# Performance work log

Hardware: AMD Instinct MI355X
Metric: run time of the kernel (lower is better)

Reference implementation:

```python
import jax, jax.numpy as jnp
import numpy as np


def _node_layer(X, Z, adj_v, T, W, b, p):
    # d_e = (Z @ p^T): per-edge scalar; multiplier = T diag(d_e) T^T  (Nv,Nv)
    d = (Z @ p.T)[:, 0]
    mult = (T * d[None, :]) @ T.T
    n = mult.shape[0]
    idx = jnp.arange(n)
    M = mult.at[idx, idx].set(1.0)           # diagonal forced to 1
    A = M * adj_v
    A = A / jnp.max(A, axis=0, keepdims=True)  # column-max normalization
    return A @ (X @ W) + b, Z


def _edge_layer(X, Z, adj_e, T, W, b, p):
    # d_v = (X @ p^T): per-node scalar; multiplier = T^T diag(d_v) T  (Ne,Ne)
    d = (X @ p.T)[:, 0]
    mult = (T.T * d[None, :]) @ T
    n = mult.shape[0]
    idx = jnp.arange(n)
    M = mult.at[idx, idx].set(1.0)
    A = M * adj_e
    A = A / jnp.max(A, axis=0, keepdims=True)
    return X, A @ (Z @ W) + b


def setup_inputs() -> dict:
    key = jax.random.key(0)
    ks = jax.random.split(key, 16)
    B, Nv, Ne = 16, 1024, 2048
    Fv, Fe, H, C = 128, 64, 128, 16
    inp = {
        "X": jax.random.normal(ks[0], (B, Nv, Fv), jnp.float32),
        "Z": jax.random.normal(ks[1], (B, Ne, Fe), jnp.float32),
        "adj_e": jax.random.uniform(ks[2], (B, Ne, Ne), jnp.float32, 0.01, 1.0),
        "adj_v": jax.random.uniform(ks[3], (B, Nv, Nv), jnp.float32, 0.01, 1.0),
        "T": jax.random.uniform(ks[4], (B, Nv, Ne), jnp.float32),
        # gc1: node layer  nfeat_v -> nhid, p over edge features
        "W1": jax.random.normal(ks[5], (Fv, H), jnp.float32) * 0.05,
        "b1": jnp.zeros((H,), jnp.float32),
        "p1": jax.random.normal(ks[6], (1, Fe), jnp.float32),
        # gc2: edge layer  nfeat_e -> nfeat_e, p over node features (nhid)
        "W2": jax.random.normal(ks[7], (Fe, Fe), jnp.float32) * 0.05,
        "b2": jnp.zeros((Fe,), jnp.float32),
        "p2": jax.random.normal(ks[8], (1, H), jnp.float32),
        # gc3: node layer  nhid -> nclass
        "W3": jax.random.normal(ks[9], (H, C), jnp.float32) * 0.05,
        "b3": jnp.zeros((C,), jnp.float32),
        "p3": jax.random.normal(ks[10], (1, Fe), jnp.float32),
    }
    return inp


def reference(X, Z, adj_e, adj_v, T, W1, b1, p1, W2, b2, p2, W3, b3, p3):
    # dropout is identity in eval mode
    def single(x, z, ae, av, t):
        x1, z1 = _node_layer(x, z, av, t, W1, b1, p1)
        x1, z1 = jax.nn.relu(x1), jax.nn.relu(z1)
        x2, z2 = _edge_layer(x1, z1, ae, t, W2, b2, p2)
        x2, z2 = jax.nn.relu(x2), jax.nn.relu(z2)
        x3, _ = _node_layer(x2, z2, av, t, W3, b3, p3)
        return x3
    return jax.vmap(single)(X, Z, adj_e, adj_v, T)  # (B, Nv, nclass)
```

## Files before the change

kernel.cpp:

```cpp
#include <hip/hip_runtime.h>
#include <hip/hip_bf16.h>
#include <stdint.h>

#define DEVI __device__ __forceinline__

typedef __bf16 bf16x8_t __attribute__((ext_vector_type(8)));
typedef float f32x4_t __attribute__((ext_vector_type(4)));
typedef unsigned short u16;

static constexpr int NBATCH = 16;
static constexpr int NV = 1024;
static constexpr int NE = 2048;
static constexpr int FV = 128;
static constexpr int FE = 64;
static constexpr int HID = 128;
static constexpr int NCLS = 16;

DEVI u16 f2bf(float f) { __hip_bfloat16 h = __float2bfloat16(f); return *reinterpret_cast<u16*>(&h); }
DEVI float bf2f(u16 u) { union { unsigned int i; float f; } x; x.i = ((unsigned int)u) << 16; return x.f; }

DEVI void gload_lds16(const void* g, void* l) {
  __builtin_amdgcn_global_load_lds(
      (const __attribute__((address_space(1))) unsigned int*)g,
      (__attribute__((address_space(3))) unsigned int*)l, 16, 0, 0);
}

__global__ void k_transpose(const float* __restrict__ T, u16* __restrict__ Tbf,
                            u16* __restrict__ Ttbf) {
  __shared__ u16 s[32][33];
  const int b = blockIdx.z;
  const int e0 = blockIdx.x * 32, v0 = blockIdx.y * 32;
  const float* Tb = T + (size_t)b * NV * NE;
  u16* T1 = Tbf + (size_t)b * NV * NE;
  u16* T2 = Ttbf + (size_t)b * NE * NV;
  const int tx = threadIdx.x & 31, ty = threadIdx.x >> 5;
  #pragma unroll
  for (int i = 0; i < 4; ++i) {
    int v = v0 + ty + i * 8;
    u16 u = f2bf(Tb[(size_t)v * NE + e0 + tx]);
    T1[(size_t)v * NE + e0 + tx] = u;
    s[ty + i * 8][tx] = u;
  }
  __syncthreads();
  #pragma unroll
  for (int i = 0; i < 4; ++i) {
    int e = e0 + ty + i * 8;
    T2[(size_t)e * NV + v0 + tx] = s[tx][ty + i * 8];
  }
}

__global__ void k_rowdot(const float* __restrict__ In, const float* __restrict__ p,
                         float* __restrict__ d, int R, int C) {
  const int b = blockIdx.y;
  const int w = threadIdx.x >> 6, l = threadIdx.x & 63;
  const int r = blockIdx.x * 4 + w;
  const float* row = In + ((size_t)b * R + r) * C;
  float s = 0.f;
  for (int c = l; c < C; c += 64) s += row[c] * p[c];
  #pragma unroll
  for (int o = 32; o; o >>= 1) s += __shfl_xor(s, o);
  if (l == 0) d[(size_t)b * R + r] = s;
}

template <bool BFIN>
__global__ void k_scale(const void* __restrict__ In, const float* __restrict__ d,
                        u16* __restrict__ Out, int K, int b0) {
  const int bi = blockIdx.y, bg = b0 + bi;
  const size_t elems = (size_t)NV * NE;
  const size_t idx = ((size_t)blockIdx.x * 256 + threadIdx.x) * 8;
  const float* dd = d + (size_t)bg * K;
  const int k = (int)(idx & (size_t)(K - 1));
  float f[8];
  if (BFIN) {
    const u16* in = (const u16*)In + (size_t)bg * elems + idx;
    uint4 raw = *(const uint4*)in;
    f[0] = bf2f(raw.x & 0xffff); f[1] = bf2f(raw.x >> 16);
    f[2] = bf2f(raw.y & 0xffff); f[3] = bf2f(raw.y >> 16);
    f[4] = bf2f(raw.z & 0xffff); f[5] = bf2f(raw.z >> 16);
    f[6] = bf2f(raw.w & 0xffff); f[7] = bf2f(raw.w >> 16);
  } else {
    const float* in = (const float*)In + (size_t)bg * elems + idx;
    float4 a0 = *(const float4*)in, a1 = *(const float4*)(in + 4);
    f[0] = a0.x; f[1] = a0.y; f[2] = a0.z; f[3] = a0.w;
    f[4] = a1.x; f[5] = a1.y; f[6] = a1.z; f[7] = a1.w;
  }
  u16 o[8];
  #pragma unroll
  for (int t = 0; t < 8; ++t) o[t] = f2bf(f[t] * dd[k + t]);
  *(uint4*)((u16*)Out + (size_t)bi * elems + idx) = *(uint4*)o;
}

__global__ __launch_bounds__(512, 2) void k_gemm256(
    const u16* __restrict__ A, size_t sA, int ldA,
    const u16* __restrict__ Bm, size_t sB, int ldB,
    int M, int K,
    const float* __restrict__ adj, u16* __restrict__ Pout, int b0) {
  extern __shared__ char smem[];
  const int gx = gridDim.x, gy = gridDim.y;
  const int total = gx * gy * gridDim.z;
  int orig = blockIdx.x + gx * (blockIdx.y + gy * blockIdx.z);
  const int cpx = total >> 3;
  int swz = (orig & 7) * cpx + (orig >> 3);
  const int bx = swz % gx;
  const int by = (swz / gx) % gy;
  const int bi = swz / (gx * gy);
  const int bg = b0 + bi;

  const u16* Ab = A + (size_t)bi * sA;
  const u16* Bb = Bm + (size_t)bg * sB;
  const int tm = by * 256, tn = bx * 256;
  const int tid = threadIdx.x, wid = tid >> 6, l = tid & 63;
  const int wr = wid >> 2, wc = wid & 3;

  const int srow = tid >> 3;
  const int scol = (((tid & 7) ^ (srow & 7)) << 3);

  const int Lx = (l & 7) << 4;
  const int colb0 = (((l >> 4) << 4)) ^ Lx;
  const int colb1 = (64 + ((l >> 4) << 4)) ^ Lx;
  const int arowb = (wr * 128 + (l & 15)) * 128;
  const int browb = (wc * 64 + (l & 15)) * 128;

  auto stage = [&](int buf, int k0) {
    char* ab = smem + (buf << 16);
    char* bb = ab + 32768;
    #pragma unroll
    for (int ld2 = 0; ld2 < 4; ++ld2) {
      gload_lds16(Ab + (size_t)(tm + ld2 * 64 + srow) * ldA + (k0 + scol),
                  ab + ld2 * 8192 + tid * 16);
      gload_lds16(Bb + (size_t)(tn + ld2 * 64 + srow) * ldB + (k0 + scol),
                  bb + ld2 * 8192 + tid * 16);
    }
  };

  f32x4_t acc[8][4];
  const f32x4_t zv = {0.f, 0.f, 0.f, 0.f};
  #pragma unroll
  for (int m = 0; m < 8; ++m)
    #pragma unroll
    for (int n = 0; n < 4; ++n) acc[m][n] = zv;

  const int NT = K >> 6;
  stage(0, 0);
  __syncthreads();

  for (int kt = 0; kt < NT; ++kt) {
    const int buf = kt & 1;
    if (kt + 1 < NT) stage(buf ^ 1, (kt + 1) << 6);
    char* abase = smem + (buf << 16);
    char* bbase = abase + 32768;
    bf16x8_t af[4][2], bfr[4][2];
    #pragma unroll
    for (int m = 0; m < 4; ++m) {
      af[m][0] = *(const bf16x8_t*)(abase + arowb + m * 2048 + colb0);
      af[m][1] = *(const bf16x8_t*)(abase + arowb + m * 2048 + colb1);
    }
    #pragma unroll
    for (int n = 0; n < 2; ++n) {
      bfr[n][0] = *(const bf16x8_t*)(bbase + browb + n * 2048 + colb0);
      bfr[n][1] = *(const bf16x8_t*)(bbase + browb + n * 2048 + colb1);
    }
    __builtin_amdgcn_s_setprio(1);
    #pragma unroll
    for (int m = 0; m < 4; ++m)
      #pragma unroll
      for (int n = 0; n < 2; ++n)
        #pragma unroll
        for (int kk = 0; kk < 2; ++kk)
          acc[m][n] = __builtin_amdgcn_mfma_f32_16x16x32_bf16(af[m][kk], bfr[n][kk], acc[m][n], 0, 0, 0);
    __builtin_amdgcn_s_setprio(0);
    #pragma unroll
    for (int n = 2; n < 4; ++n) {
      bfr[n][0] = *(const bf16x8_t*)(bbase + browb + n * 2048 + colb0);
      bfr[n][1] = *(const bf16x8_t*)(bbase + browb + n * 2048 + colb1);
    }
    __builtin_amdgcn_s_setprio(1);
    #pragma unroll
    for (int m = 0; m < 4; ++m)
      #pragma unroll
      for (int n = 2; n < 4; ++n)
        #pragma unroll
        for (int kk = 0; kk < 2; ++kk)
          acc[m][n] = __builtin_amdgcn_mfma_f32_16x16x32_bf16(af[m][kk], bfr[n][kk], acc[m][n], 0, 0, 0);
    __builtin_amdgcn_s_setprio(0);
    #pragma unroll
    for (int m = 0; m < 4; ++m) {
      af[m][0] = *(const bf16x8_t*)(abase + arowb + (m + 4) * 2048 + colb0);
      af[m][1] = *(const bf16x8_t*)(abase + arowb + (m + 4) * 2048 + colb1);
    }
    __builtin_amdgcn_s_setprio(1);
    #pragma unroll
    for (int m = 0; m < 4; ++m)
      #pragma unroll
      for (int n = 2; n < 4; ++n)
        #pragma unroll
        for (int kk = 0; kk < 2; ++kk)
          acc[m + 4][n] = __builtin_amdgcn_mfma_f32_16x16x32_bf16(af[m][kk], bfr[n][kk], acc[m + 4][n], 0, 0, 0);
    __builtin_amdgcn_s_setprio(0);
    __builtin_amdgcn_s_setprio(1);
    #pragma unroll
    for (int m = 0; m < 4; ++m)
      #pragma unroll
      for (int n = 0; n < 2; ++n)
        #pragma unroll
        for (int kk = 0; kk < 2; ++kk)
          acc[m + 4][n] = __builtin_amdgcn_mfma_f32_16x16x32_bf16(af[m][kk], bfr[n][kk], acc[m + 4][n], 0, 0, 0);
    __builtin_amdgcn_s_setprio(0);
    __syncthreads();
  }

  const float* adjb = adj + (size_t)bg * M * M;
  u16* Pb = Pout + (size_t)bi * (size_t)M * M;
  #pragma unroll
  for (int m = 0; m < 8; ++m)
    #pragma unroll
    for (int n = 0; n < 4; ++n)
      #pragma unroll
      for (int q = 0; q < 4; ++q) {
        int row = tm + wr * 128 + m * 16 + (l >> 4) * 4 + q;
        int col = tn + wc * 64 + n * 16 + (l & 15);
        float v = acc[m][n][q];
        if (row == col) v = 1.0f;
        v *= adjb[(size_t)row * M + col];
        Pb[(size_t)row * M + col] = f2bf(v);
      }
}

template <int EPI>
__global__ __launch_bounds__(256) void k_gemm(
    const u16* __restrict__ A, size_t sA, int ldA,
    const u16* __restrict__ Bm, size_t sB, int ldB,
    int M, int K, int Nrows, int Ncols,
    const float* __restrict__ bias, float* __restrict__ Fout, int b0) {
  __shared__ __align__(16) u16 As[2][128 * 32];
  __shared__ __align__(16) u16 Bs[2][128 * 32];
  const int bi = blockIdx.z, bg = b0 + bi;
  const u16* Ab = A + (size_t)bi * sA;
  const u16* Bb = Bm + (size_t)bg * sB;
  const int tm = blockIdx.y * 128, tn = blockIdx.x * 128;
  const int tid = threadIdx.x, w = tid >> 6, l = tid & 63;
  const int wm = (w >> 1) * 64, wn = (w & 1) * 64;
  const int lr = l & 15, kg = (l >> 4) * 8;
  const int chunk = l & 3;
  int arow[2], brow[2];
  #pragma unroll
  for (int i = 0; i < 2; ++i) {
    int r = (i * 4 + w) * 16 + (l >> 2);
    arow[i] = tm + r;
    int rb = tn + r;
    brow[i] = rb < Nrows ? rb : Nrows - 1;
  }
  f32x4_t acc[4][4];
  const f32x4_t zv = {0.f, 0.f, 0.f, 0.f};
  #pragma unroll
  for (int m = 0; m < 4; ++m)
    #pragma unroll
    for (int n = 0; n < 4; ++n) acc[m][n] = zv;

  auto stage = [&](int buf, int k0) {
    #pragma unroll
    for (int i = 0; i < 2; ++i) {
      gload_lds16(Ab + (size_t)arow[i] * ldA + k0 + chunk * 8,
                  (char*)As[buf] + (i * 4 + w) * 1024);
      gload_lds16(Bb + (size_t)brow[i] * ldB + k0 + chunk * 8,
                  (char*)Bs[buf] + (i * 4 + w) * 1024);
    }
  };

  const int nsteps = K >> 5;
  stage(0, 0);
  __syncthreads();
  for (int s = 0; s < nsteps; ++s) {
    const int cur = s & 1;
    if (s + 1 < nsteps) stage(cur ^ 1, (s + 1) << 5);
    bf16x8_t af[4], bfr[4];
    #pragma unroll
    for (int m = 0; m < 4; ++m) af[m] = *(const bf16x8_t*)&As[cur][(wm + m * 16 + lr) * 32 + kg];
    #pragma unroll
    for (int n = 0; n < 4; ++n) bfr[n] = *(const bf16x8_t*)&Bs[cur][(wn + n * 16 + lr) * 32 + kg];
    #pragma unroll
    for (int m = 0; m < 4; ++m)
      #pragma unroll
      for (int n = 0; n < 4; ++n)
        acc[m][n] = __builtin_amdgcn_mfma_f32_16x16x32_bf16(af[m], bfr[n], acc[m][n], 0, 0, 0);
    __syncthreads();
  }

  float* Ob = Fout + (size_t)bg * M * Ncols;
  #pragma unroll
  for (int m = 0; m < 4; ++m)
    #pragma unroll
    for (int n = 0; n < 4; ++n)
      #pragma unroll
      for (int q = 0; q < 4; ++q) {
        int row = tm + wm + m * 16 + (l >> 4) * 4 + q;
        int col = tn + wn + n * 16 + lr;
        if (col < Ncols) {
          float v = acc[m][n][q] + bias[col];
          if (EPI == 1) v = fmaxf(v, 0.f);
          Ob[(size_t)row * Ncols + col] = v;
        }
      }
}

__global__ void k_colmax(const u16* __restrict__ P, unsigned int* __restrict__ c,
                         int M, int N, int rowsPer, int b0) {
  const int bi = blockIdx.z, bg = b0 + bi;
  const u16* Pb = P + (size_t)bi * (size_t)M * N;
  const int j = (blockIdx.x * 256 + threadIdx.x) * 4;
  const int r0 = blockIdx.y * rowsPer;
  float m0 = 0.f, m1 = 0.f, m2 = 0.f, m3 = 0.f;
  for (int i = r0; i < r0 + rowsPer; ++i) {
    uint2 v = *(const uint2*)(Pb + (size_t)i * N + j);
    m0 = fmaxf(m0, bf2f(v.x & 0xffff)); m1 = fmaxf(m1, bf2f(v.x >> 16));
    m2 = fmaxf(m2, bf2f(v.y & 0xffff)); m3 = fmaxf(m3, bf2f(v.y >> 16));
  }
  unsigned int* cb = c + (size_t)bg * N;
  atomicMax(cb + j + 0, __float_as_uint(m0));
  atomicMax(cb + j + 1, __float_as_uint(m1));
  atomicMax(cb + j + 2, __float_as_uint(m2));
  atomicMax(cb + j + 3, __float_as_uint(m3));
}

template <bool RELU_IN>
__global__ __launch_bounds__(256) void k_smallgemm(
    const float* __restrict__ X, size_t sX, int Kd,
    const float* __restrict__ W, int Cc,
    const float* __restrict__ cmax, u16* __restrict__ YT, size_t sY,
    int Nj, int b0) {
  __shared__ float Xs[64][129];
  __shared__ float Ws[128][33];
  const int bg = b0 + blockIdx.y;
  const float* Xb = X + (size_t)bg * sX;
  const int j0 = blockIdx.x * 64;
  const int tid = threadIdx.x;
  for (int idx = tid; idx < 64 * (Kd / 4); idx += 256) {
    int r = idx / (Kd / 4), q = idx % (Kd / 4);
    float4 v = *(const float4*)(Xb + (size_t)(j0 + r) * Kd + q * 4);
    if (RELU_IN) {
      v.x = fmaxf(v.x, 0.f); v.y = fmaxf(v.y, 0.f);
      v.z = fmaxf(v.z, 0.f); v.w = fmaxf(v.w, 0.f);
    }
    Xs[r][q * 4 + 0] = v.x; Xs[r][q * 4 + 1] = v.y;
    Xs[r][q * 4 + 2] = v.z; Xs[r][q * 4 + 3] = v.w;
  }
  const int r = tid & 63, cg = tid >> 6;
  const float rinv = 1.0f / cmax[(size_t)bg * Nj + j0 + r];
  for (int c0 = 0; c0 < Cc; c0 += 32) {
    __syncthreads();
    for (int idx = tid; idx < Kd * 32; idx += 256) {
      int k = idx >> 5, c = c0 + (idx & 31);
      Ws[k][idx & 31] = (c < Cc) ? W[(size_t)k * Cc + c] : 0.f;
    }
    __syncthreads();
    float acc[8] = {0.f, 0.f, 0.f, 0.f, 0.f, 0.f, 0.f, 0.f};
    for (int k = 0; k < Kd; ++k) {
      float xv = Xs[r][k];
      #pragma unroll
      for (int cc = 0; cc < 8; ++cc) acc[cc] += xv * Ws[k][cg * 8 + cc];
    }
    #pragma unroll
    for (int cc = 0; cc < 8; ++cc) {
      int c = c0 + cg * 8 + cc;
      if (c < Cc) YT[(size_t)bg * sY + (size_t)c * Nj + j0 + r] = f2bf(acc[cc] * rinv);
    }
  }
}

extern "C" void kernel_launch(void* const* d_in, const int* in_sizes, int n_in,
                              void* d_out, int out_size, void* d_ws, size_t ws_size,
                              hipStream_t stream) {
  const float* X    = (const float*)d_in[0];
  const float* Z    = (const float*)d_in[1];
  const float* adje = (const float*)d_in[2];
  const float* adjv = (const float*)d_in[3];
  const float* T    = (const float*)d_in[4];
  const float* W1   = (const float*)d_in[5];
  const float* b1   = (const float*)d_in[6];
  const float* p1   = (const float*)d_in[7];
  const float* W2   = (const float*)d_in[8];
  const float* b2   = (const float*)d_in[9];
  const float* p2   = (const float*)d_in[10];
  const float* W3   = (const float*)d_in[11];
  const float* b3   = (const float*)d_in[12];
  const float* p3   = (const float*)d_in[13];
  float* out = (float*)d_out;
  (void)in_sizes; (void)n_in; (void)out_size;

  hipFuncSetAttribute(reinterpret_cast<const void*>(k_gemm256),
                      hipFuncAttributeMaxDynamicSharedMemorySize, 131072);

  char* ws = (char*)d_ws;
  size_t off = 0;
  auto alloc = [&](size_t n) -> char* {
    char* p = ws + off; off = (off + n + 255) & ~(size_t)255; return p;
  };
  u16* Tbf    = (u16*)alloc((size_t)NBATCH * NV * NE * 2);
  u16* Ttbf   = (u16*)alloc((size_t)NBATCH * NE * NV * 2);
  float* dbuf = (float*)alloc((size_t)NBATCH * NE * 4);
  float* cbuf = (float*)alloc((size_t)NBATCH * NE * 4);
  u16* YT     = (u16*)alloc((size_t)NBATCH * NE * 64 * 2);
  float* x1   = (float*)alloc((size_t)NBATCH * NV * HID * 4);
  float* z2   = (float*)alloc((size_t)NBATCH * NE * FE * 4);
  const size_t needA = (size_t)NBATCH * NV * NE * 2;
  const size_t needP = (size_t)NBATCH * NE * NE * 2;
  const bool full = (ws_size >= off + needA + needP + 1024);
  const int nb = full ? NBATCH : 1;
  u16* Asc = (u16*)alloc(full ? needA : (size_t)NV * NE * 2);
  u16* P   = (u16*)alloc(full ? needP : (size_t)NE * NE * 2);

  const dim3 blk(256, 1, 1);
  const dim3 blk512(512, 1, 1);
  const size_t cbytes = (size_t)NBATCH * NE * 4;

  k_transpose<<<dim3(NE / 32, NV / 32, NBATCH), blk, 0, stream>>>(T, Tbf, Ttbf);

  k_rowdot<<<dim3(NE / 4, NBATCH), blk, 0, stream>>>(Z, p1, dbuf, NE, FE);
  for (int b0 = 0; b0 < NBATCH; b0 += nb) {
    k_scale<false><<<dim3((NV * NE) / 2048, nb), blk, 0, stream>>>(T, dbuf, Asc, NE, b0);
    k_gemm256<<<dim3(NV / 256, NV / 256, nb), blk512, 131072, stream>>>(
        Asc, (size_t)NV * NE, NE, Tbf, (size_t)NV * NE, NE, NV, NE, adjv, P, b0);
    hipMemsetAsync(cbuf, 0, cbytes, stream);
    k_colmax<<<dim3(NV / 1024, NV / 32, nb), blk, 0, stream>>>(
        P, (unsigned int*)cbuf, NV, NV, 32, b0);
    k_smallgemm<false><<<dim3(NV / 64, nb), blk, 0, stream>>>(
        X, (size_t)NV * FV, FV, W1, HID, cbuf, YT, (size_t)NV * HID, NV, b0);
    k_gemm<1><<<dim3(1, NV / 128, nb), blk, 0, stream>>>(
        P, (size_t)NV * NV, NV, YT, (size_t)NV * HID, NV,
        NV, NV, HID, HID, b1, x1, b0);
  }
  k_rowdot<<<dim3(NV / 4, NBATCH), blk, 0, stream>>>(x1, p2, dbuf, NV, HID);
  for (int b0 = 0; b0 < NBATCH; b0 += nb) {
    k_scale<true><<<dim3((NE * NV) / 2048, nb), blk, 0, stream>>>(Ttbf, dbuf, Asc, NV, b0);
    k_gemm256<<<dim3(NE / 256, NE / 256, nb), blk512, 131072, stream>>>(
        Asc, (size_t)NE * NV, NV, Ttbf, (size_t)NE * NV, NV, NE, NV, adje, P, b0);
    hipMemsetAsync(cbuf, 0, cbytes, stream);
    k_colmax<<<dim3(NE / 1024, NE / 64, nb), blk, 0, stream>>>(
        P, (unsigned int*)cbuf, NE, NE, 64, b0);
    k_smallgemm<true><<<dim3(NE / 64, nb), blk, 0, stream>>>(
        Z, (size_t)NE * FE, FE, W2, FE, cbuf, YT, (size_t)NE * FE, NE, b0);
    k_gemm<1><<<dim3(1, NE / 128, nb), blk, 0, stream>>>(
        P, (size_t)NE * NE, NE, YT, (size_t)NE * FE, NE,
        NE, NE, FE, FE, b2, z2, b0);
  }
  k_rowdot<<<dim3(NE / 4, NBATCH), blk, 0, stream>>>(z2, p3, dbuf, NE, FE);
  for (int b0 = 0; b0 < NBATCH; b0 += nb) {
    k_scale<false><<<dim3((NV * NE) / 2048, nb), blk, 0, stream>>>(T, dbuf, Asc, NE, b0);
    k_gemm256<<<dim3(NV / 256, NV / 256, nb), blk512, 131072, stream>>>(
        Asc, (size_t)NV * NE, NE, Tbf, (size_t)NV * NE, NE, NV, NE, adjv, P, b0);
    hipMemsetAsync(cbuf, 0, cbytes, stream);
    k_colmax<<<dim3(NV / 1024, NV / 32, nb), blk, 0, stream>>>(
        P, (unsigned int*)cbuf, NV, NV, 32, b0);
    k_smallgemm<false><<<dim3(NV / 64, nb), blk, 0, stream>>>(
        x1, (size_t)NV * HID, HID, W3, NCLS, cbuf, YT, (size_t)NV * NCLS, NV, b0);
    k_gemm<2><<<dim3(1, NV / 128, nb), blk, 0, stream>>>(
        P, (size_t)NV * NV, NV, YT, (size_t)NV * NCLS, NV,
        NV, NV, NCLS, NCLS, b3, out, b0);
  }
}
```

Baseline: 759.1 us.

## Split GEMM tile into quadrant phases with staged prefetch and fine-grained barriers

After: 734.9 us. 3.2% less time.

```diff
diff --git a/kernel.cpp b/kernel.cpp
--- a/kernel.cpp
+++ b/kernel.cpp
@@ -90,12 +90,38 @@
   *(uint4*)((u16*)Out + (size_t)bi * elems + idx) = *(uint4*)o;
 }
 
+#define LDA8(MH) \
+  _Pragma("unroll") \
+  for (int m = 0; m < 4; ++m) { \
+    const char* pA = abase + ((MH) * 128 + wr * 64 + m * 16 + lr) * 128; \
+    af[m][0] = *(const bf16x8_t*)(pA + colb0); \
+    af[m][1] = *(const bf16x8_t*)(pA + colb1); \
+  }
+#define LDB4(BF, NH) \
+  _Pragma("unroll") \
+  for (int n = 0; n < 2; ++n) { \
+    const char* pB = bbase + ((NH) * 128 + wc * 32 + n * 16 + lr) * 128; \
+    BF[n][0] = *(const bf16x8_t*)(pB + colb0); \
+    BF[n][1] = *(const bf16x8_t*)(pB + colb1); \
+  }
+#define MFMA_QUAD(MH, NH, BF) \
+  __builtin_amdgcn_s_setprio(1); \
+  _Pragma("unroll") \
+  for (int m = 0; m < 4; ++m) \
+    _Pragma("unroll") \
+    for (int n = 0; n < 2; ++n) \
+      _Pragma("unroll") \
+      for (int kk = 0; kk < 2; ++kk) \
+        acc[(MH) * 4 + m][(NH) * 2 + n] = __builtin_amdgcn_mfma_f32_16x16x32_bf16( \
+            af[m][kk], BF[n][kk], acc[(MH) * 4 + m][(NH) * 2 + n], 0, 0, 0); \
+  __builtin_amdgcn_s_setprio(0);
+
 __global__ __launch_bounds__(512, 2) void k_gemm256(
     const u16* __restrict__ A, size_t sA, int ldA,
     const u16* __restrict__ Bm, size_t sB, int ldB,
     int M, int K,
     const float* __restrict__ adj, u16* __restrict__ Pout, int b0) {
-  extern __shared__ char smem[];
+  extern __shared__ __align__(16) char smem[];
   const int gx = gridDim.x, gy = gridDim.y;
   const int total = gx * gy * gridDim.z;
   int orig = blockIdx.x + gx * (blockIdx.y + gy * blockIdx.z);
@@ -111,26 +137,22 @@
   const int tm = by * 256, tn = bx * 256;
   const int tid = threadIdx.x, wid = tid >> 6, l = tid & 63;
   const int wr = wid >> 2, wc = wid & 3;
-
-  const int srow = tid >> 3;
-  const int scol = (((tid & 7) ^ (srow & 7)) << 3);
-
+  const int lr = l & 15;
   const int Lx = (l & 7) << 4;
   const int colb0 = (((l >> 4) << 4)) ^ Lx;
   const int colb1 = (64 + ((l >> 4) << 4)) ^ Lx;
-  const int arowb = (wr * 128 + (l & 15)) * 128;
-  const int browb = (wc * 64 + (l & 15)) * 128;
-
-  auto stage = [&](int buf, int k0) {
-    char* ab = smem + (buf << 16);
-    char* bb = ab + 32768;
-    #pragma unroll
-    for (int ld2 = 0; ld2 < 4; ++ld2) {
-      gload_lds16(Ab + (size_t)(tm + ld2 * 64 + srow) * ldA + (k0 + scol),
-                  ab + ld2 * 8192 + tid * 16);
-      gload_lds16(Bb + (size_t)(tn + ld2 * 64 + srow) * ldB + (k0 + scol),
-                  bb + ld2 * 8192 + tid * 16);
-    }
+  const int srow = tid >> 3;
+  const int scol = (((tid & 7) ^ (srow & 7)) << 3);
+
+  auto stageA = [&](char* ab, int k0, int pa) {
+    const int rho = pa * 64 + srow;
+    const int row = ((rho >> 6) & 1) * 128 + (rho >> 7) * 64 + (rho & 63);
+    gload_lds16(Ab + (size_t)(tm + row) * ldA + (k0 + scol), ab + pa * 8192 + tid * 16);
+  };
+  auto stageB = [&](char* bb, int k0, int pb) {
+    const int rho = pb * 64 + srow;
+    const int row = ((rho >> 5) & 3) * 64 + (rho >> 7) * 32 + (rho & 31);
+    gload_lds16(Bb + (size_t)(tn + row) * ldB + (k0 + scol), bb + pb * 8192 + tid * 16);
   };
 
   f32x4_t acc[8][4];
@@ -139,74 +161,61 @@
   for (int m = 0; m < 8; ++m)
     #pragma unroll
     for (int n = 0; n < 4; ++n) acc[m][n] = zv;
+  bf16x8_t af[4][2], blo[2][2], bhi[2][2];
 
   const int NT = K >> 6;
-  stage(0, 0);
-  __syncthreads();
+  {
+    char* ab = smem; char* bb = smem + 32768;
+    stageA(ab, 0, 0); stageA(ab, 0, 1);
+    stageB(bb, 0, 0); stageB(bb, 0, 1);
+    stageB(bb, 0, 2); stageB(bb, 0, 3);
+    stageA(ab, 0, 2); stageA(ab, 0, 3);
+  }
+  asm volatile("s_waitcnt vmcnt(4)" ::: "memory");
+  __builtin_amdgcn_s_barrier();
 
   for (int kt = 0; kt < NT; ++kt) {
-    const int buf = kt & 1;
-    if (kt + 1 < NT) stage(buf ^ 1, (kt + 1) << 6);
-    char* abase = smem + (buf << 16);
+    char* abase = smem + ((kt & 1) << 16);
     char* bbase = abase + 32768;
-    bf16x8_t af[4][2], bfr[4][2];
-    #pragma unroll
-    for (int m = 0; m < 4; ++m) {
-      af[m][0] = *(const bf16x8_t*)(abase + arowb + m * 2048 + colb0);
-      af[m][1] = *(const bf16x8_t*)(abase + arowb + m * 2048 + colb1);
-    }
-    #pragma unroll
-    for (int n = 0; n < 2; ++n) {
-      bfr[n][0] = *(const bf16x8_t*)(bbase + browb + n * 2048 + colb0);
-      bfr[n][1] = *(const bf16x8_t*)(bbase + browb + n * 2048 + colb1);
-    }
-    __builtin_amdgcn_s_setprio(1);
-    #pragma unroll
-    for (int m = 0; m < 4; ++m)
-      #pragma unroll
-      for (int n = 0; n < 2; ++n)
-        #pragma unroll
-        for (int kk = 0; kk < 2; ++kk)
-          acc[m][n] = __builtin_amdgcn_mfma_f32_16x16x32_bf16(af[m][kk], bfr[n][kk], acc[m][n], 0, 0, 0);
-    __builtin_amdgcn_s_setprio(0);
-    #pragma unroll
-    for (int n = 2; n < 4; ++n) {
-      bfr[n][0] = *(const bf16x8_t*)(bbase + browb + n * 2048 + colb0);
-      bfr[n][1] = *(const bf16x8_t*)(bbase + browb + n * 2048 + colb1);
-    }
-    __builtin_amdgcn_s_setprio(1);
-    #pragma unroll
-    for (int m = 0; m < 4; ++m)
-      #pragma unroll
-      for (int n = 2; n < 4; ++n)
-        #pragma unroll
-        for (int kk = 0; kk < 2; ++kk)
-          acc[m][n] = __builtin_amdgcn_mfma_f32_16x16x32_bf16(af[m][kk], bfr[n][kk], acc[m][n], 0, 0, 0);
-    __builtin_amdgcn_s_setprio(0);
-    #pragma unroll
-    for (int m = 0; m < 4; ++m) {
-      af[m][0] = *(const bf16x8_t*)(abase + arowb + (m + 4) * 2048 + colb0);
-      af[m][1] = *(const bf16x8_t*)(abase + arowb + (m + 4) * 2048 + colb1);
-    }
-    __builtin_amdgcn_s_setprio(1);
-    #pragma unroll
-    for (int m = 0; m < 4; ++m)
-      #pragma unroll
-      for (int n = 2; n < 4; ++n)
-        #pragma unroll
-        for (int kk = 0; kk < 2; ++kk)
-          acc[m + 4][n] = __builtin_amdgcn_mfma_f32_16x16x32_bf16(af[m][kk], bfr[n][kk], acc[m + 4][n], 0, 0, 0);
-    __builtin_amdgcn_s_setprio(0);
-    __builtin_amdgcn_s_setprio(1);
-    #pragma unroll
-    for (int m = 0; m < 4; ++m)
-      #pragma unroll
-      for (int n = 0; n < 2; ++n)
-        #pragma unroll
-        for (int kk = 0; kk < 2; ++kk)
-          acc[m + 4][n] = __builtin_amdgcn_mfma_f32_16x16x32_bf16(af[m][kk], bfr[n][kk], acc[m + 4][n], 0, 0, 0);
-    __builtin_amdgcn_s_setprio(0);
-    __syncthreads();
+    char* nab = smem + (((kt & 1) ^ 1) << 16);
+    char* nbb = nab + 32768;
+    const int nk0 = (kt + 1) << 6;
+    const bool pre = (kt + 1 < NT);
+
+    LDA8(0);
+    LDB4(blo, 0);
+    if (pre) { stageA(nab, nk0, 0); stageA(nab, nk0, 1); }
+    __builtin_amdgcn_s_barrier();
+    asm volatile("s_waitcnt lgkmcnt(0)" ::: "memory");
+    __builtin_amdgcn_sched_barrier(0);
+    MFMA_QUAD(0, 0, blo);
+    if (pre) asm volatile("s_waitcnt vmcnt(4)" ::: "memory");
+    else     asm volatile("s_waitcnt vmcnt(2)" ::: "memory");
+    __builtin_amdgcn_s_barrier();
+
+    LDB4(bhi, 1);
+    if (pre) { stageB(nbb, nk0, 0); stageB(nbb, nk0, 1); }
+    __builtin_amdgcn_s_barrier();
+    asm volatile("s_waitcnt lgkmcnt(0)" ::: "memory");
+    __builtin_amdgcn_sched_barrier(0);
+    MFMA_QUAD(0, 1, bhi);
+    if (pre) asm volatile("s_waitcnt vmcnt(4)" ::: "memory");
+    else     asm volatile("s_waitcnt vmcnt(0)" ::: "memory");
+    __builtin_amdgcn_s_barrier();
+
+    LDA8(1);
+    if (pre) { stageB(nbb, nk0, 2); stageB(nbb, nk0, 3); }
+    __builtin_amdgcn_s_barrier();
+    asm volatile("s_waitcnt lgkmcnt(0)" ::: "memory");
+    __builtin_amdgcn_sched_barrier(0);
+    MFMA_QUAD(1, 0, blo);
+    __builtin_amdgcn_s_barrier();
+
+    if (pre) { stageA(nab, nk0, 2); stageA(nab, nk0, 3); }
+    __builtin_amdgcn_s_barrier();
+    MFMA_QUAD(1, 1, bhi);
+    if (pre) asm volatile("s_waitcnt vmcnt(4)" ::: "memory");
+    __builtin_amdgcn_s_barrier();
   }
 
   const float* adjb = adj + (size_t)bg * M * M;
@@ -417,7 +426,7 @@
 
   k_rowdot<<<dim3(NE / 4, NBATCH), blk, 0, stream>>>(Z, p1, dbuf, NE, FE);
   for (int b0 = 0; b0 < NBATCH; b0 += nb) {
-    k_scale<false><<<dim3((NV * NE) / 2048, nb), blk, 0, stream>>>(T, dbuf, Asc, NE, b0);
+    k_scale<true><<<dim3((NV * NE) / 2048, nb), blk, 0, stream>>>(Tbf, dbuf, Asc, NE, b0);
     k_gemm256<<<dim3(NV / 256, NV / 256, nb), blk512, 131072, stream>>>(
         Asc, (size_t)NV * NE, NE, Tbf, (size_t)NV * NE, NE, NV, NE, adjv, P, b0);
     hipMemsetAsync(cbuf, 0, cbytes, stream);
@@ -445,7 +454,7 @@
   }
   k_rowdot<<<dim3(NE / 4, NBATCH), blk, 0, stream>>>(z2, p3, dbuf, NE, FE);
   for (int b0 = 0; b0 < NBATCH; b0 += nb) {
-    k_scale<false><<<dim3((NV * NE) / 2048, nb), blk, 0, stream>>>(T, dbuf, Asc, NE, b0);
+    k_scale<true><<<dim3((NV * NE) / 2048, nb), blk, 0, stream>>>(Tbf, dbuf, Asc, NE, b0);
     k_gemm256<<<dim3(NV / 256, NV / 256, nb), blk512, 131072, stream>>>(
         Asc, (size_t)NV * NE, NE, Tbf, (size_t)NV * NE, NE, NV, NE, adjv, P, b0);
     hipMemsetAsync(cbuf, 0, cbytes, stream);
```

## Fuse column-max into GEMM epilogue and scaling into transpose, add narrow PY GEMM

Applied to the files above, without the earlier changes.

Result: faster. 659.7 us (-13.1%).

```diff
diff --git a/kernel.cpp b/kernel.cpp
--- a/kernel.cpp
+++ b/kernel.cpp
@@ -25,8 +25,10 @@
       (__attribute__((address_space(3))) unsigned int*)l, 16, 0, 0);
 }
 
+template <bool WRITE_ASC>
 __global__ void k_transpose(const float* __restrict__ T, u16* __restrict__ Tbf,
-                            u16* __restrict__ Ttbf) {
+                            u16* __restrict__ Ttbf, const float* __restrict__ d1,
+                            u16* __restrict__ Asc1) {
   __shared__ u16 s[32][33];
   const int b = blockIdx.z;
   const int e0 = blockIdx.x * 32, v0 = blockIdx.y * 32;
@@ -34,11 +36,15 @@
   u16* T1 = Tbf + (size_t)b * NV * NE;
   u16* T2 = Ttbf + (size_t)b * NE * NV;
   const int tx = threadIdx.x & 31, ty = threadIdx.x >> 5;
+  float dv = 0.f;
+  if (WRITE_ASC) dv = d1[(size_t)b * NE + e0 + tx];
   #pragma unroll
   for (int i = 0; i < 4; ++i) {
     int v = v0 + ty + i * 8;
-    u16 u = f2bf(Tb[(size_t)v * NE + e0 + tx]);
+    float f = Tb[(size_t)v * NE + e0 + tx];
+    u16 u = f2bf(f);
     T1[(size_t)v * NE + e0 + tx] = u;
+    if (WRITE_ASC) Asc1[(size_t)b * NV * NE + (size_t)v * NE + e0 + tx] = f2bf(f * dv);
     s[ty + i * 8][tx] = u;
   }
   __syncthreads();
@@ -62,28 +68,20 @@
   if (l == 0) d[(size_t)b * R + r] = s;
 }
 
-template <bool BFIN>
-__global__ void k_scale(const void* __restrict__ In, const float* __restrict__ d,
+__global__ void k_scale(const u16* __restrict__ In, const float* __restrict__ d,
                         u16* __restrict__ Out, int K, int b0) {
   const int bi = blockIdx.y, bg = b0 + bi;
   const size_t elems = (size_t)NV * NE;
   const size_t idx = ((size_t)blockIdx.x * 256 + threadIdx.x) * 8;
   const float* dd = d + (size_t)bg * K;
   const int k = (int)(idx & (size_t)(K - 1));
+  const u16* in = In + (size_t)bg * elems + idx;
+  uint4 raw = *(const uint4*)in;
   float f[8];
-  if (BFIN) {
-    const u16* in = (const u16*)In + (size_t)bg * elems + idx;
-    uint4 raw = *(const uint4*)in;
-    f[0] = bf2f(raw.x & 0xffff); f[1] = bf2f(raw.x >> 16);
-    f[2] = bf2f(raw.y & 0xffff); f[3] = bf2f(raw.y >> 16);
-    f[4] = bf2f(raw.z & 0xffff); f[5] = bf2f(raw.z >> 16);
-    f[6] = bf2f(raw.w & 0xffff); f[7] = bf2f(raw.w >> 16);
-  } else {
-    const float* in = (const float*)In + (size_t)bg * elems + idx;
-    float4 a0 = *(const float4*)in, a1 = *(const float4*)(in + 4);
-    f[0] = a0.x; f[1] = a0.y; f[2] = a0.z; f[3] = a0.w;
-    f[4] = a1.x; f[5] = a1.y; f[6] = a1.z; f[7] = a1.w;
-  }
+  f[0] = bf2f(raw.x & 0xffff); f[1] = bf2f(raw.x >> 16);
+  f[2] = bf2f(raw.y & 0xffff); f[3] = bf2f(raw.y >> 16);
+  f[4] = bf2f(raw.z & 0xffff); f[5] = bf2f(raw.z >> 16);
+  f[6] = bf2f(raw.w & 0xffff); f[7] = bf2f(raw.w >> 16);
   u16 o[8];
   #pragma unroll
   for (int t = 0; t < 8; ++t) o[t] = f2bf(f[t] * dd[k + t]);
@@ -94,8 +92,9 @@
     const u16* __restrict__ A, size_t sA, int ldA,
     const u16* __restrict__ Bm, size_t sB, int ldB,
     int M, int K,
-    const float* __restrict__ adj, u16* __restrict__ Pout, int b0) {
-  extern __shared__ char smem[];
+    const float* __restrict__ adj, u16* __restrict__ Pout,
+    float* __restrict__ pmax, int b0) {
+  extern __shared__ __align__(16) char smem[];
   const int gx = gridDim.x, gy = gridDim.y;
   const int total = gx * gy * gridDim.z;
   int orig = blockIdx.x + gx * (blockIdx.y + gy * blockIdx.z);
@@ -211,6 +210,7 @@
 
   const float* adjb = adj + (size_t)bg * M * M;
   u16* Pb = Pout + (size_t)bi * (size_t)M * M;
+  float vmax[4] = {0.f, 0.f, 0.f, 0.f};
   #pragma unroll
   for (int m = 0; m < 8; ++m)
     #pragma unroll
@@ -222,8 +222,39 @@
         float v = acc[m][n][q];
         if (row == col) v = 1.0f;
         v *= adjb[(size_t)row * M + col];
+        vmax[n] = fmaxf(vmax[n], v);
         Pb[(size_t)row * M + col] = f2bf(v);
       }
+  #pragma unroll
+  for (int n = 0; n < 4; ++n) {
+    vmax[n] = fmaxf(vmax[n], __shfl_xor(vmax[n], 16));
+    vmax[n] = fmaxf(vmax[n], __shfl_xor(vmax[n], 32));
+  }
+  float* red = (float*)smem;
+  if (l < 16) {
+    #pragma unroll
+    for (int n = 0; n < 4; ++n)
+      red[((wr * 4 + wc) * 4 + n) * 16 + l] = vmax[n];
+  }
+  __syncthreads();
+  if (wr == 0 && l < 16) {
+    #pragma unroll
+    for (int n = 0; n < 4; ++n) {
+      float a = red[((0 * 4 + wc) * 4 + n) * 16 + l];
+      float b = red[((1 * 4 + wc) * 4 + n) * 16 + l];
+      pmax[((size_t)bi * gy + by) * M + tn + wc * 64 + n * 16 + l] = fmaxf(a, b);
+    }
+  }
+}
+
+__global__ void k_colmax2(const float* __restrict__ pmax, float* __restrict__ c,
+                          int N, int G, int b0) {
+  const int bi = blockIdx.y, bg = b0 + bi;
+  const int j = blockIdx.x * 256 + threadIdx.x;
+  const float* pb = pmax + (size_t)bi * G * N;
+  float m = 0.f;
+  for (int g = 0; g < G; ++g) m = fmaxf(m, pb[(size_t)g * N + j]);
+  c[(size_t)bg * N + j] = m;
 }
 
 template <int EPI>
@@ -303,23 +334,77 @@
       }
 }
 
-__global__ void k_colmax(const u16* __restrict__ P, unsigned int* __restrict__ c,
-                         int M, int N, int rowsPer, int b0) {
+template <int EPI>
+__global__ __launch_bounds__(256) void k_gemmPY(
+    const u16* __restrict__ A, size_t sA, int ldA,
+    const u16* __restrict__ Bm, size_t sB,
+    int M, int K, int Ncols,
+    const float* __restrict__ bias, float* __restrict__ Fout, int b0) {
+  __shared__ __align__(16) u16 As[2][128 * 32];
+  __shared__ __align__(16) u16 Bs[2][64 * 32];
   const int bi = blockIdx.z, bg = b0 + bi;
-  const u16* Pb = P + (size_t)bi * (size_t)M * N;
-  const int j = (blockIdx.x * 256 + threadIdx.x) * 4;
-  const int r0 = blockIdx.y * rowsPer;
-  float m0 = 0.f, m1 = 0.f, m2 = 0.f, m3 = 0.f;
-  for (int i = r0; i < r0 + rowsPer; ++i) {
-    uint2 v = *(const uint2*)(Pb + (size_t)i * N + j);
-    m0 = fmaxf(m0, bf2f(v.x & 0xffff)); m1 = fmaxf(m1, bf2f(v.x >> 16));
-    m2 = fmaxf(m2, bf2f(v.y & 0xffff)); m3 = fmaxf(m3, bf2f(v.y >> 16));
-  }
-  unsigned int* cb = c + (size_t)bg * N;
-  atomicMax(cb + j + 0, __float_as_uint(m0));
-  atomicMax(cb + j + 1, __float_as_uint(m1));
-  atomicMax(cb + j + 2, __float_as_uint(m2));
-  atomicMax(cb + j + 3, __float_as_uint(m3));
+  const u16* Ab = A + (size_t)bi * sA;
+  const u16* Bb = Bm + (size_t)bg * sB;
+  const int tm = blockIdx.y * 128;
+  const int tid = threadIdx.x, w = tid >> 6, l = tid & 63;
+  const int wm = (w >> 1) * 64, wn = (w & 1) * 32;
+  const int lr = l & 15, kg = (l >> 4) * 8;
+  const int chunk = l & 3;
+  int arow[2];
+  #pragma unroll
+  for (int i = 0; i < 2; ++i) arow[i] = tm + (i * 4 + w) * 16 + (l >> 2);
+  const int brow = w * 16 + (l >> 2);
+
+  f32x4_t acc[4][2];
+  const f32x4_t zv = {0.f, 0.f, 0.f, 0.f};
+  #pragma unroll
+  for (int m = 0; m < 4; ++m)
+    #pragma unroll
+    for (int n = 0; n < 2; ++n) acc[m][n] = zv;
+
+  auto stage = [&](int buf, int k0) {
+    #pragma unroll
+    for (int i = 0; i < 2; ++i)
+      gload_lds16(Ab + (size_t)arow[i] * ldA + k0 + chunk * 8,
+                  (char*)As[buf] + (i * 4 + w) * 1024);
+    gload_lds16(Bb + (size_t)brow * ldA  + k0 + chunk * 8,
+                (char*)Bs[buf] + tid * 16);
+  };
+
+  const int nsteps = K >> 5;
+  stage(0, 0);
+  __syncthreads();
+  for (int s = 0; s < nsteps; ++s) {
+    const int cur = s & 1;
+    if (s + 1 < nsteps) stage(cur ^ 1, (s + 1) << 5);
+    bf16x8_t af[4], bfr[2];
+    #pragma unroll
+    for (int m = 0; m < 4; ++m) af[m] = *(const bf16x8_t*)&As[cur][(wm + m * 16 + lr) * 32 + kg];
+    #pragma unroll
+    for (int n = 0; n < 2; ++n) bfr[n] = *(const bf16x8_t*)&Bs[cur][(wn + n * 16 + lr) * 32 + kg];
+    #pragma unroll
+    for (int m = 0; m < 4; ++m)
+      #pragma unroll
+      for (int n = 0; n < 2; ++n)
+        acc[m][n] = __builtin_amdgcn_mfma_f32_16x16x32_bf16(af[m], bfr[n], acc[m][n], 0, 0, 0);
+    __syncthreads();
+  }
+
+  float* Ob = Fout + (size_t)bg * M * Ncols;
+  #pragma unroll
+  for (int m = 0; m < 4; ++m)
+    #pragma unroll
+    for (int n = 0; n < 2; ++n)
+      #pragma unroll
+      for (int q = 0; q < 4; ++q) {
+        int row = tm + wm + m * 16 + (l >> 4) * 4 + q;
+        int col = wn + n * 16 + lr;
+        if (col < Ncols) {
+          float v = acc[m][n][q] + bias[col];
+          if (EPI == 1) v = fmaxf(v, 0.f);
+          Ob[(size_t)row * Ncols + col] = v;
+        }
+      }
 }
 
 template <bool RELU_IN>
@@ -399,6 +484,7 @@
   u16* Ttbf   = (u16*)alloc((size_t)NBATCH * NE * NV * 2);
   float* dbuf = (float*)alloc((size_t)NBATCH * NE * 4);
   float* cbuf = (float*)alloc((size_t)NBATCH * NE * 4);
+  float* pmax = (float*)alloc((size_t)NBATCH * 8 * NE * 4);
   u16* YT     = (u16*)alloc((size_t)NBATCH * NE * 64 * 2);
   float* x1   = (float*)alloc((size_t)NBATCH * NV * HID * 4);
   float* z2   = (float*)alloc((size_t)NBATCH * NE * FE * 4);
@@ -411,18 +497,21 @@
 
   const dim3 blk(256, 1, 1);
   const dim3 blk512(512, 1, 1);
-  const size_t cbytes = (size_t)NBATCH * NE * 4;
-
-  k_transpose<<<dim3(NE / 32, NV / 32, NBATCH), blk, 0, stream>>>(T, Tbf, Ttbf);
 
   k_rowdot<<<dim3(NE / 4, NBATCH), blk, 0, stream>>>(Z, p1, dbuf, NE, FE);
+  if (full)
+    k_transpose<true><<<dim3(NE / 32, NV / 32, NBATCH), blk, 0, stream>>>(
+        T, Tbf, Ttbf, dbuf, Asc);
+  else
+    k_transpose<false><<<dim3(NE / 32, NV / 32, NBATCH), blk, 0, stream>>>(
+        T, Tbf, Ttbf, nullptr, nullptr);
+
   for (int b0 = 0; b0 < NBATCH; b0 += nb) {
-    k_scale<false><<<dim3((NV * NE) / 2048, nb), blk, 0, stream>>>(T, dbuf, Asc, NE, b0);
+    if (!full)
+      k_scale<<<dim3((NV * NE) / 2048, nb), blk, 0, stream>>>(Tbf, dbuf, Asc, NE, b0);
     k_gemm256<<<dim3(NV / 256, NV / 256, nb), blk512, 131072, stream>>>(
-        Asc, (size_t)NV * NE, NE, Tbf, (size_t)NV * NE, NE, NV, NE, adjv, P, b0);
-    hipMemsetAsync(cbuf, 0, cbytes, stream);
-    k_colmax<<<dim3(NV / 1024, NV / 32, nb), blk, 0, stream>>>(
-        P, (unsigned int*)cbuf, NV, NV, 32, b0);
+        Asc, (size_t)NV * NE, NE, Tbf, (size_t)NV * NE, NE, NV, NE, adjv, P, pmax, b0);
+    k_colmax2<<<dim3(NV / 256, nb), blk, 0, stream>>>(pmax, cbuf, NV, NV / 256, b0);
     k_smallgemm<false><<<dim3(NV / 64, nb), blk, 0, stream>>>(
         X, (size_t)NV * FV, FV, W1, HID, cbuf, YT, (size_t)NV * HID, NV, b0);
     k_gemm<1><<<dim3(1, NV / 128, nb), blk, 0, stream>>>(
@@ -431,30 +520,26 @@
   }
   k_rowdot<<<dim3(NV / 4, NBATCH), blk, 0, stream>>>(x1, p2, dbuf, NV, HID);
   for (int b0 = 0; b0 < NBATCH; b0 += nb) {
-    k_scale<true><<<dim3((NE * NV) / 2048, nb), blk, 0, stream>>>(Ttbf, dbuf, Asc, NV, b0);
+    k_scale<<<dim3((NE * NV) / 2048, nb), blk, 0, stream>>>(Ttbf, dbuf, Asc, NV, b0);
     k_gemm256<<<dim3(NE / 256, NE / 256, nb), blk512, 131072, stream>>>(
-        Asc, (size_t)NE * NV, NV, Ttbf, (size_t)NE * NV, NV, NE, NV, adje, P, b0);
-    hipMemsetAsync(cbuf, 0, cbytes, stream);
-    k_colmax<<<dim3(NE / 1024, NE / 64, nb), blk, 0, stream>>>(
-        P, (unsigned int*)cbuf, NE, NE, 64, b0);
+        Asc, (size_t)NE * NV, NV, Ttbf, (size_t)NE * NV, NV, NE, NV, adje, P, pmax, b0);
+    k_colmax2<<<dim3(NE / 256, nb), blk, 0, stream>>>(pmax, cbuf, NE, NE / 256, b0);
     k_smallgemm<true><<<dim3(NE / 64, nb), blk, 0, stream>>>(
         Z, (size_t)NE * FE, FE, W2, FE, cbuf, YT, (size_t)NE * FE, NE, b0);
-    k_gemm<1><<<dim3(1, NE / 128, nb), blk, 0, stream>>>(
-        P, (size_t)NE * NE, NE, YT, (size_t)NE * FE, NE,
-        NE, NE, FE, FE, b2, z2, b0);
+    k_gemmPY<1><<<dim3(1, NE / 128, nb), blk, 0, stream>>>(
+        P, (size_t)NE * NE, NE, YT, (size_t)NE * FE,
+        NE, NE, FE, b2, z2, b0);
   }
   k_rowdot<<<dim3(NE / 4, NBATCH), blk, 0, stream>>>(z2, p3, dbuf, NE, FE);
   for (int b0 = 0; b0 < NBATCH; b0 += nb) {
-    k_scale<false><<<dim3((NV * NE) / 2048, nb), blk, 0, stream>>>(T, dbuf, Asc, NE, b0);
+    k_scale<<<dim3((NV * NE) / 2048, nb), blk, 0, stream>>>(Tbf, dbuf, Asc, NE, b0);
     k_gemm256<<<dim3(NV / 256, NV / 256, nb), blk512, 131072, stream>>>(
-        Asc, (size_t)NV * NE, NE, Tbf, (size_t)NV * NE, NE, NV, NE, adjv, P, b0);
-    hipMemsetAsync(cbuf, 0, cbytes, stream);
-    k_colmax<<<dim3(NV / 1024, NV / 32, nb), blk, 0, stream>>>(
-        P, (unsigned int*)cbuf, NV, NV, 32, b0);
+        Asc, (size_t)NV * NE, NE, Tbf, (size_t)NV * NE, NE, NV, NE, adjv, P, pmax, b0);
+    k_colmax2<<<dim3(NV / 256, nb), blk, 0, stream>>>(pmax, cbuf, NV, NV / 256, b0);
     k_smallgemm<false><<<dim3(NV / 64, nb), blk, 0, stream>>>(
         x1, (size_t)NV * HID, HID, W3, NCLS, cbuf, YT, (size_t)NV * NCLS, NV, b0);
-    k_gemm<2><<<dim3(1, NV / 128, nb), blk, 0, stream>>>(
-        P, (size_t)NV * NV, NV, YT, (size_t)NV * NCLS, NV,
-        NV, NV, NCLS, NCLS, b3, out, b0);
-  }
-}
+    k_gemmPY<2><<<dim3(1, NV / 128, nb), blk, 0, stream>>>(
+        P, (size_t)NV * NV, NV, YT, (size_t)NV * NCLS,
+        NV, NV, NCLS, b3, out, b0);
+  }
+}
```
